# Kernel tuning notes

Hardware: AMD Instinct MI355X
Metric: run time of the kernel (lower is better)

The kernel has to match this reference:

```python
import jax, jax.numpy as jnp
import numpy as np

B, C_IN, H, W = 8, 32, 64, 64
C = 64  # num_channels


def setup_inputs() -> dict:
    key = jax.random.key(0)
    ks = jax.random.split(key, 9)
    s_in = 1.0 / np.sqrt(C_IN)
    s_c = 1.0 / np.sqrt(C)
    return {
        "x": jax.random.normal(ks[0], (B, C_IN, H, W), dtype=jnp.float32),
        "wq": jax.random.uniform(ks[1], (C, C_IN), jnp.float32, -s_in, s_in),
        "bq": jax.random.uniform(ks[2], (C,), jnp.float32, -s_in, s_in),
        "wk": jax.random.uniform(ks[3], (C, C_IN), jnp.float32, -s_in, s_in),
        "bk": jax.random.uniform(ks[4], (C,), jnp.float32, -s_in, s_in),
        "wv": jax.random.uniform(ks[5], (C, C_IN), jnp.float32, -s_in, s_in),
        "bv": jax.random.uniform(ks[6], (C,), jnp.float32, -s_in, s_in),
        "wo": jax.random.uniform(ks[7], (C_IN, C), jnp.float32, -s_c, s_c),
        "bo": jax.random.uniform(ks[8], (C_IN,), jnp.float32, -s_c, s_c),
    }


def reference(x, wq, bq, wk, bk, wv, bv, wo, bo):
    b, c_in, h, w = x.shape
    n = h * w
    # 1x1 convs == per-pixel linear projections; produce (B, N, C) directly
    q = (jnp.einsum('bchw,oc->bhwo', x, wq) + bq).reshape(b, n, -1)
    k = (jnp.einsum('bchw,oc->bhwo', x, wk) + bk).reshape(b, n, -1)
    v = (jnp.einsum('bchw,oc->bhwo', x, wv) + bv).reshape(b, n, -1)
    # unscaled attention over spatial positions (no 1/sqrt(d) in original)
    scores = jnp.einsum('bnc,bmc->bnm', q, k)  # (B, N, N)
    attn = jax.nn.softmax(scores, axis=-1)
    out = jnp.einsum('bnm,bmc->bnc', attn, v)  # (B, N, C)
    out = out.reshape(b, h, w, -1)
    out = jnp.einsum('bhwc,oc->bohw', out, wo) + bo[None, :, None, None]
    return out + x
```

## Files before the change

kernel.cpp:

```cpp
#include <hip/hip_runtime.h>
#include <hip/hip_bf16.h>

#define CIN    32
#define NPIX   4096
#define DIM    64
#define LOG2E  1.4426950408889634f

#if __has_builtin(__builtin_amdgcn_exp2f)
#define EXP2(x) __builtin_amdgcn_exp2f(x)
#else
#define EXP2(x) exp2f(x)
#endif

typedef float  f32x4  __attribute__((ext_vector_type(4)));
typedef float  f32x16 __attribute__((ext_vector_type(16)));
typedef short  s16x8  __attribute__((ext_vector_type(8)));

#define ZERO16 {0.f,0.f,0.f,0.f,0.f,0.f,0.f,0.f,0.f,0.f,0.f,0.f,0.f,0.f,0.f,0.f}

__device__ __forceinline__ f32x16 mfma32(s16x8 a, s16x8 b, f32x16 c) {
    return __builtin_amdgcn_mfma_f32_32x32x16_bf16(a, b, c, 0, 0, 0);
}


__global__ __launch_bounds__(256) void qkv_proj(
    const float* __restrict__ x,
    const float* __restrict__ wq, const float* __restrict__ bq,
    const float* __restrict__ wk, const float* __restrict__ bk,
    const float* __restrict__ wv, const float* __restrict__ bv,
    __hip_bfloat16* __restrict__ qb, __hip_bfloat16* __restrict__ kb,
    __hip_bfloat16* __restrict__ vb)
{
    __shared__ float Xs[CIN][64];
    __shared__ float wT[3][CIN][DIM];

    const int tid = threadIdx.x;
    const int b   = blockIdx.y;
    const int bx  = blockIdx.x;
    const int n0  = bx * 64;

    for (int i = tid; i < 3 * CIN * DIM; i += 256) {
        int m = i >> 11, r = i & 2047, c = r >> 6, o = r & 63;
        const float* wsrc = (m == 0) ? wq : (m == 1) ? wk : wv;
        float wv0 = wsrc[o * CIN + c];
        wT[m][c][o] = (m == 0) ? wv0 * LOG2E : wv0;
    }
    for (int i = tid * 4; i < CIN * 64; i += 1024) {
        int c = i >> 6, p = i & 63;
        *(f32x4*)&Xs[c][p] = *(const f32x4*)&x[((size_t)b * CIN + c) * NPIX + n0 + p];
    }
    __syncthreads();

    const int w    = tid >> 6;
    const int lane = tid & 63;
    const int l16  = lane >> 2;
    const int quad = lane & 3;

    const int T  = bx * 4 + w;
    const int px = T * 16 + l16;

    float aq[2][8], ak[2][8];
    #pragma unroll
    for (int kb2 = 0; kb2 < 2; kb2++) {
        f32x4 bq0 = *(const f32x4*)&bq[kb2 * 32 + quad * 8];
        f32x4 bq1 = *(const f32x4*)&bq[kb2 * 32 + quad * 8 + 4];
        f32x4 bk0 = *(const f32x4*)&bk[kb2 * 32 + quad * 8];
        f32x4 bk1 = *(const f32x4*)&bk[kb2 * 32 + quad * 8 + 4];
        #pragma unroll
        for (int j = 0; j < 4; j++) {
            aq[kb2][j] = bq0[j] * LOG2E; aq[kb2][j + 4] = bq1[j] * LOG2E;
            ak[kb2][j] = bk0[j];         ak[kb2][j + 4] = bk1[j];
        }
    }
    #pragma unroll 8
    for (int c = 0; c < CIN; c++) {
        const float xc = Xs[c][w * 16 + l16];
        #pragma unroll
        for (int kb2 = 0; kb2 < 2; kb2++) {
            f32x4 q0 = *(const f32x4*)&wT[0][c][kb2 * 32 + quad * 8];
            f32x4 q1 = *(const f32x4*)&wT[0][c][kb2 * 32 + quad * 8 + 4];
            f32x4 k0 = *(const f32x4*)&wT[1][c][kb2 * 32 + quad * 8];
            f32x4 k1 = *(const f32x4*)&wT[1][c][kb2 * 32 + quad * 8 + 4];
            #pragma unroll
            for (int j = 0; j < 4; j++) {
                aq[kb2][j]     += xc * q0[j];
                aq[kb2][j + 4] += xc * q1[j];
                ak[kb2][j]     += xc * k0[j];
                ak[kb2][j + 4] += xc * k1[j];
            }
        }
    }
    {
        const int s   = px >> 5;
        const int key = px & 31;
        #pragma unroll
        for (int kb2 = 0; kb2 < 2; kb2++) {
            union { s16x8 v; __hip_bfloat16 h[8]; } pq, pk;
            #pragma unroll
            for (int j = 0; j < 8; j++) {
                pq.h[j] = __float2bfloat16(aq[kb2][j]);
                pk.h[j] = __float2bfloat16(ak[kb2][j]);
            }
            *(s16x8*)(qb + ((size_t)b * NPIX + px) * DIM + kb2 * 32 + quad * 8) = pq.v;
            const int kt = kb2 * 2 + (quad >> 1);
            const int h  = quad & 1;
            const size_t koff = (size_t)b * 262144
                + ((size_t)(s * 4 + kt) * 64 + h * 32 + key) * 8;
            *(s16x8*)(kb + koff) = pk.v;
        }
    }

    const int ch = w * 16 + l16;
    float av[2][8];
    {
        const float bvc = bv[ch];
        #pragma unroll
        for (int kh = 0; kh < 2; kh++)
            #pragma unroll
            for (int j = 0; j < 8; j++) av[kh][j] = bvc;
    }
    #pragma unroll 8
    for (int c = 0; c < CIN; c++) {
        const float wvc = wT[2][c][ch];
        f32x4 x0 = *(const f32x4*)&Xs[c][quad * 8];
        f32x4 x1 = *(const f32x4*)&Xs[c][quad * 8 + 4];
        f32x4 x2 = *(const f32x4*)&Xs[c][32 + quad * 8];
        f32x4 x3 = *(const f32x4*)&Xs[c][32 + quad * 8 + 4];
        #pragma unroll
        for (int j = 0; j < 4; j++) {
            av[0][j]     += x0[j] * wvc;
            av[0][j + 4] += x1[j] * wvc;
            av[1][j]     += x2[j] * wvc;
            av[1][j + 4] += x3[j] * wvc;
        }
    }
    #pragma unroll
    for (int kh = 0; kh < 2; kh++) {
        const int s = bx * 2 + kh;
        #pragma unroll
        for (int h = 0; h < 2; h++) {
            union { unsigned long long u; __hip_bfloat16 hh[4]; } pv;
            #pragma unroll
            for (int j = 0; j < 4; j++) pv.hh[j] = __float2bfloat16(av[kh][h * 4 + j]);
            const size_t voff = (size_t)b * 262144
                + (size_t)(s * 4 + (ch >> 5) * 2 + (quad >> 1)) * 512
                + (size_t)(h * 32 + (ch & 31)) * 8
                + 4 * (quad & 1);
            *(unsigned long long*)(vb + voff) = pv.u;
        }
    }
}

__global__ __launch_bounds__(512, 4) void attn_fused(
    const __hip_bfloat16* __restrict__ qb,
    const __hip_bfloat16* __restrict__ kbf,
    const __hip_bfloat16* __restrict__ vbf,
    const float* __restrict__ wo, const float* __restrict__ bo,
    const float* __restrict__ x, float* __restrict__ y)
{
    __shared__ __align__(16) char sm[2][8][4096];
    __shared__ float LRED2[3][2][32];

    float (*REDq)[2][64][33] = (float (*)[2][64][33])&sm[0][0][0];

    const int tid  = threadIdx.x;
    const int w    = tid >> 6;
    const int g    = w >> 2;
    const int kq   = w & 3;
    const int lane = tid & 63;
    const int q    = lane & 31;
    const int hl   = lane >> 5;
    const int b    = blockIdx.x;
    const int row0 = blockIdx.y * 64 + g * 32;

    s16x8 qf[4];
    #pragma unroll
    for (int kt = 0; kt < 4; kt++)
        qf[kt] = *(const s16x8*)(qb + ((size_t)b * NPIX + row0 + q) * DIM
                                 + kt * 16 + hl * 8);

    f32x16 o0 = ZERO16, o1 = ZERO16;
    float lsacc = 0.f;

    const char* stbase = ((w >> 2) ? (const char*)vbf : (const char*)kbf)
                       + (size_t)b * 524288
                       + (size_t)(w & 3) * 131072
                       + (size_t)lane * 16;
    char* std0 = &sm[0][w][lane * 16];
    char* std1 = &sm[1][w][lane * 16];

    #pragma unroll
    for (int i = 0; i < 4; i++)
        *(f32x4*)(std0 + i * 1024) = *(const f32x4*)(stbase + i * 1024);
    __syncthreads();

    int cur = 0;
    for (int p = 0; p < 32; ++p) {
        const char* Kl = sm[cur][kq];
        s16x8 kf[4];
        #pragma unroll
        for (int i = 0; i < 4; i++)
            kf[i] = *(const s16x8*)(Kl + i * 1024 + lane * 16);

        const size_t srcoff = (size_t)((p < 31) ? p + 1 : 31) * 4096;
        f32x4 r0 = *(const f32x4*)(stbase + srcoff);
        f32x4 r1 = *(const f32x4*)(stbase + srcoff + 1024);
        f32x4 r2 = *(const f32x4*)(stbase + srcoff + 2048);
        f32x4 r3 = *(const f32x4*)(stbase + srcoff + 3072);

        __builtin_amdgcn_s_setprio(1);
        f32x16 sA = ZERO16, sB = ZERO16;
        sA = mfma32(kf[0], qf[0], sA);
        sB = mfma32(kf[2], qf[2], sB);
        sA = mfma32(kf[1], qf[1], sA);
        sB = mfma32(kf[3], qf[3], sB);
        __builtin_amdgcn_s_setprio(0);

        union { s16x8 v; __hip_bfloat16 h8[8]; } p0, p1;
        #pragma unroll
        for (int j = 0; j < 8; j++) {
            float e0 = EXP2(sA[j] + sB[j]);
            float e1 = EXP2(sA[8 + j] + sB[8 + j]);
            lsacc += e0 + e1;
            p0.h8[j] = __float2bfloat16(e0);
            p1.h8[j] = __float2bfloat16(e1);
        }

        const char* Vl = sm[cur][4 + kq];
        s16x8 vv[4];
        #pragma unroll
        for (int i = 0; i < 4; i++)
            vv[i] = *(const s16x8*)(Vl + i * 1024 + lane * 16);

        __builtin_amdgcn_s_setprio(1);
        o0 = mfma32(vv[0], p0.v, o0);
        o1 = mfma32(vv[2], p0.v, o1);
        o0 = mfma32(vv[1], p1.v, o0);
        o1 = mfma32(vv[3], p1.v, o1);
        __builtin_amdgcn_s_setprio(0);

        char* dst = cur ? std0 : std1;
        *(f32x4*)(dst)        = r0;
        *(f32x4*)(dst + 1024) = r1;
        *(f32x4*)(dst + 2048) = r2;
        *(f32x4*)(dst + 3072) = r3;
        __syncthreads();
        cur ^= 1;
    }

    lsacc += __shfl_xor(lsacc, 32, 64);

    if (kq != 0) {
        #pragma unroll
        for (int i = 0; i < 16; i++) {
            const int rr = (i & 3) + 8 * (i >> 2) + 4 * hl;
            REDq[kq - 1][g][rr][q]      = o0[i];
            REDq[kq - 1][g][32 + rr][q] = o1[i];
        }
        if (hl == 0) LRED2[kq - 1][g][q] = lsacc;
    }
    __syncthreads();

    if (kq == 0) {
        #pragma unroll
        for (int sl = 0; sl < 3; sl++) {
            lsacc += LRED2[sl][g][q];
            #pragma unroll
            for (int i = 0; i < 16; i++) {
                const int rr = (i & 3) + 8 * (i >> 2) + 4 * hl;
                o0[i] += REDq[sl][g][rr][q];
                o1[i] += REDq[sl][g][32 + rr][q];
            }
        }
        const float inv = 1.0f / lsacc;

        s16x8 pbo[4];
        #pragma unroll
        for (int gg = 0; gg < 4; gg++) {
            union { s16x8 v; __hip_bfloat16 h8[8]; } pk;
            #pragma unroll
            for (int j = 0; j < 8; j++) {
                const float vv2 = (gg < 2) ? o0[(gg & 1) * 8 + j] : o1[(gg & 1) * 8 + j];
                pk.h8[j] = __float2bfloat16(vv2 * inv);
            }
            pbo[gg] = pk.v;
        }

        s16x8 aw[4];
        #pragma unroll
        for (int gg = 0; gg < 4; gg++) {
            f32x4 w0 = *(const f32x4*)(wo + (size_t)q * DIM + gg * 16 + hl * 4);
            f32x4 w1 = *(const f32x4*)(wo + (size_t)q * DIM + gg * 16 + 8 + hl * 4);
            union { s16x8 v; __hip_bfloat16 h8[8]; } wf;
            #pragma unroll
            for (int j = 0; j < 4; j++) {
                wf.h8[j]     = __float2bfloat16(w0[j]);
                wf.h8[4 + j] = __float2bfloat16(w1[j]);
            }
            aw[gg] = wf.v;
        }

        f32x16 d = ZERO16;
        #pragma unroll
        for (int gg = 0; gg < 4; gg++)
            d = mfma32(aw[gg], pbo[gg], d);

        #pragma unroll
        for (int i = 0; i < 16; i++) {
            const int out = (i & 3) + 8 * (i >> 2) + 4 * hl;
            const int row = row0 + q;
            const size_t xi = ((size_t)b * CIN + out) * NPIX + row;
            y[xi] = d[i] + bo[out] + x[xi];
        }
    }
}

extern "C" void kernel_launch(void* const* d_in, const int* in_sizes, int n_in,
                              void* d_out, int out_size, void* d_ws, size_t ws_size,
                              hipStream_t stream)
{
    const float* x  = (const float*)d_in[0];
    const float* wq = (const float*)d_in[1];
    const float* bq = (const float*)d_in[2];
    const float* wk = (const float*)d_in[3];
    const float* bk = (const float*)d_in[4];
    const float* wv = (const float*)d_in[5];
    const float* bv = (const float*)d_in[6];
    const float* wo = (const float*)d_in[7];
    const float* bo = (const float*)d_in[8];
    float* y = (float*)d_out;

    char* ws = (char*)d_ws;
    __hip_bfloat16* qb = (__hip_bfloat16*)(ws);
    __hip_bfloat16* kb = (__hip_bfloat16*)(ws + (4u << 20));
    __hip_bfloat16* vb = (__hip_bfloat16*)(ws + (8u << 20));

    qkv_proj<<<dim3(64, 8), dim3(256), 0, stream>>>(x, wq, bq, wk, bk, wv, bv, qb, kb, vb);
    attn_fused<<<dim3(8, 64), dim3(512), 0, stream>>>(qb, kb, vb, wo, bo, x, y);
}
```

Before: 134.8 us.

## Load V fragments directly from global and stage only K through LDS

V tiles are now read directly from global memory into registers each iteration, and only K goes through the double-buffered LDS stage, with all eight waves cooperating on K. This halves LDS staging traffic and per-iteration LDS writes. It also merges the two split score accumulators into one serial MFMA chain. The cost is exposed global-load latency for V inside the loop and a longer dependent MFMA chain for the scores.

Measured after the change: 131.9 us. -2.2%, faster.

```diff
diff --git a/kernel.cpp b/kernel.cpp
--- a/kernel.cpp
+++ b/kernel.cpp
@@ -158,10 +158,11 @@
     const float* __restrict__ wo, const float* __restrict__ bo,
     const float* __restrict__ x, float* __restrict__ y)
 {
-    __shared__ __align__(16) char sm[2][8][4096];
+    __shared__ __align__(16) char smraw[50688];
     __shared__ float LRED2[3][2][32];
 
-    float (*REDq)[2][64][33] = (float (*)[2][64][33])&sm[0][0][0];
+    char (*smK)[4][4096]     = (char (*)[4][4096])smraw;
+    float (*REDq)[2][64][33] = (float (*)[2][64][33])smraw;
 
     const int tid  = threadIdx.x;
     const int w    = tid >> 6;
@@ -182,55 +183,53 @@
     f32x16 o0 = ZERO16, o1 = ZERO16;
     float lsacc = 0.f;
 
-    const char* stbase = ((w >> 2) ? (const char*)vbf : (const char*)kbf)
-                       + (size_t)b * 524288
-                       + (size_t)(w & 3) * 131072
-                       + (size_t)lane * 16;
-    char* std0 = &sm[0][w][lane * 16];
-    char* std1 = &sm[1][w][lane * 16];
-
-    #pragma unroll
-    for (int i = 0; i < 4; i++)
-        *(f32x4*)(std0 + i * 1024) = *(const f32x4*)(stbase + i * 1024);
+    const char* kst = (const char*)kbf + (size_t)b * 524288
+                    + (size_t)(w >> 1) * 131072
+                    + (size_t)(w & 1) * 2048 + (size_t)lane * 16;
+    char* std0 = &smK[0][w >> 1][(w & 1) * 2048 + lane * 16];
+    char* std1 = &smK[1][w >> 1][(w & 1) * 2048 + lane * 16];
+
+    const char* vbase = (const char*)vbf + (size_t)b * 524288
+                      + (size_t)kq * 131072 + (size_t)lane * 16;
+
+    *(f32x4*)(std0)        = *(const f32x4*)(kst);
+    *(f32x4*)(std0 + 1024) = *(const f32x4*)(kst + 1024);
     __syncthreads();
 
     int cur = 0;
     for (int p = 0; p < 32; ++p) {
-        const char* Kl = sm[cur][kq];
+        s16x8 vv[4];
+        #pragma unroll
+        for (int i = 0; i < 4; i++)
+            vv[i] = *(const s16x8*)(vbase + (size_t)p * 4096 + i * 1024);
+
+        const char* Kl = smK[cur][kq];
         s16x8 kf[4];
         #pragma unroll
         for (int i = 0; i < 4; i++)
             kf[i] = *(const s16x8*)(Kl + i * 1024 + lane * 16);
 
-        const size_t srcoff = (size_t)((p < 31) ? p + 1 : 31) * 4096;
-        f32x4 r0 = *(const f32x4*)(stbase + srcoff);
-        f32x4 r1 = *(const f32x4*)(stbase + srcoff + 1024);
-        f32x4 r2 = *(const f32x4*)(stbase + srcoff + 2048);
-        f32x4 r3 = *(const f32x4*)(stbase + srcoff + 3072);
+        const size_t so = (size_t)((p < 31) ? p + 1 : 31) * 4096;
+        f32x4 r0 = *(const f32x4*)(kst + so);
+        f32x4 r1 = *(const f32x4*)(kst + so + 1024);
 
         __builtin_amdgcn_s_setprio(1);
-        f32x16 sA = ZERO16, sB = ZERO16;
-        sA = mfma32(kf[0], qf[0], sA);
-        sB = mfma32(kf[2], qf[2], sB);
-        sA = mfma32(kf[1], qf[1], sA);
-        sB = mfma32(kf[3], qf[3], sB);
+        f32x16 s = ZERO16;
+        s = mfma32(kf[0], qf[0], s);
+        s = mfma32(kf[1], qf[1], s);
+        s = mfma32(kf[2], qf[2], s);
+        s = mfma32(kf[3], qf[3], s);
         __builtin_amdgcn_s_setprio(0);
 
         union { s16x8 v; __hip_bfloat16 h8[8]; } p0, p1;
         #pragma unroll
         for (int j = 0; j < 8; j++) {
-            float e0 = EXP2(sA[j] + sB[j]);
-            float e1 = EXP2(sA[8 + j] + sB[8 + j]);
+            float e0 = EXP2(s[j]);
+            float e1 = EXP2(s[8 + j]);
             lsacc += e0 + e1;
             p0.h8[j] = __float2bfloat16(e0);
             p1.h8[j] = __float2bfloat16(e1);
         }
-
-        const char* Vl = sm[cur][4 + kq];
-        s16x8 vv[4];
-        #pragma unroll
-        for (int i = 0; i < 4; i++)
-            vv[i] = *(const s16x8*)(Vl + i * 1024 + lane * 16);
 
         __builtin_amdgcn_s_setprio(1);
         o0 = mfma32(vv[0], p0.v, o0);
@@ -242,8 +241,6 @@
         char* dst = cur ? std0 : std1;
         *(f32x4*)(dst)        = r0;
         *(f32x4*)(dst + 1024) = r1;
-        *(f32x4*)(dst + 2048) = r2;
-        *(f32x4*)(dst + 3072) = r3;
         __syncthreads();
         cur ^= 1;
     }
```
